# Kernel optimization log

Measured on AMD Instinct MI355X. Metric: run time of the kernel, lower is better.

## Reference

```python
import jax, jax.numpy as jnp
import numpy as np

EMBED_DIM = 256
H = 80
W = 80
N_HEADS = 8
N_POINTS = 4
B = 8


def sine_pe(C, h, w):
    # LoFTR-style PositionEncodingSine, returns [1, C, h, w]
    y_pos = jnp.cumsum(jnp.ones((h, w), jnp.float32), axis=0)[None]
    x_pos = jnp.cumsum(jnp.ones((h, w), jnp.float32), axis=1)[None]
    div = jnp.exp(jnp.arange(0, C // 2, 2, dtype=jnp.float32) * (-np.log(10000.0) / (C // 2)))[:, None, None]
    pe = jnp.zeros((C, h, w), jnp.float32)
    pe = pe.at[0::4].set(jnp.sin(x_pos * div))
    pe = pe.at[1::4].set(jnp.cos(x_pos * div))
    pe = pe.at[2::4].set(jnp.sin(y_pos * div))
    pe = pe.at[3::4].set(jnp.cos(y_pos * div))
    return pe[None]


def make_reference_points(h, w):
    # Faithful to the original (W-major flatten, (col, row) stacking)
    gr = np.linspace(0, 1, w)
    gc = np.linspace(0, 1, h)
    R, Cg = np.meshgrid(gr, gc, indexing='ij')  # (w, h)
    ref = np.stack((Cg, R), -1).reshape(-1, 2)  # [w*h, 2]
    return jnp.asarray(ref, jnp.float32)


def setup_inputs():
    key = jax.random.key(0)
    ks = jax.random.split(key, 8)
    C = EMBED_DIM
    s = 1.0 / np.sqrt(C)
    return {
        'query': jax.random.normal(ks[0], (B, C, H, W), jnp.float32),
        'value': jax.random.normal(ks[1], (B, C, H, W), jnp.float32),
        'W_value': jax.random.normal(ks[2], (C, C), jnp.float32) * s,
        'b_value': jnp.zeros((C,), jnp.float32),
        'W_off': jax.random.normal(ks[3], (C, N_HEADS * N_POINTS * 2), jnp.float32) * 0.01,
        'b_off': jax.random.normal(ks[4], (N_HEADS * N_POINTS * 2,), jnp.float32) * 0.5,
        'W_attn': jax.random.normal(ks[5], (C, N_HEADS * N_POINTS), jnp.float32) * s,
        'b_attn': jnp.zeros((N_HEADS * N_POINTS,), jnp.float32),
        'W_out': jax.random.normal(ks[6], (C, C), jnp.float32) * s,
        'b_out': jnp.zeros((C,), jnp.float32),
    }


def _deform_attn_core(q, v, ref, W_off, b_off, W_attn, b_attn):
    # q: [B, Nq, C] queries; v: [B, H*W, C] projected values; ref: [Nq, 2]
    Bq, Nq, C = q.shape
    hd = C // N_HEADS
    off = (q @ W_off + b_off).reshape(Bq, Nq, N_HEADS, N_POINTS, 2)
    aw = jax.nn.softmax((q @ W_attn + b_attn).reshape(Bq, Nq, N_HEADS, N_POINTS), axis=-1)
    norm = jnp.array([W, H], jnp.float32)  # offset normalizer (W, H), num_levels=1
    loc = ref[None, :, None, None, :] + off / norm  # [B, Nq, Hn, P, 2], normalized (x, y)
    loc = loc.transpose(0, 2, 1, 3, 4)  # [B, Hn, Nq, P, 2]
    # grid_sample(align_corners=False, padding_mode='zeros'): pixel = loc*size - 0.5
    x = loc[..., 0] * W - 0.5
    y = loc[..., 1] * H - 0.5
    x0f = jnp.floor(x); y0f = jnp.floor(y)
    wx = x - x0f; wy = y - y0f
    x0 = x0f.astype(jnp.int32); y0 = y0f.astype(jnp.int32)
    vh = v.reshape(Bq, H * W, N_HEADS, hd).transpose(0, 2, 1, 3)  # [B, Hn, HW, hd]

    def gather(ix, iy):
        valid = (ix >= 0) & (ix < W) & (iy >= 0) & (iy < H)
        idx = jnp.clip(iy, 0, H - 1) * W + jnp.clip(ix, 0, W - 1)  # [B, Hn, Nq, P]
        g = jnp.take_along_axis(vh, idx.reshape(Bq, N_HEADS, -1, 1), axis=2)
        return g.reshape(Bq, N_HEADS, Nq, N_POINTS, hd) * valid[..., None].astype(v.dtype)

    samp = (gather(x0, y0) * ((1 - wx) * (1 - wy))[..., None]
            + gather(x0 + 1, y0) * (wx * (1 - wy))[..., None]
            + gather(x0, y0 + 1) * ((1 - wx) * wy)[..., None]
            + gather(x0 + 1, y0 + 1) * (wx * wy)[..., None])  # [B, Hn, Nq, P, hd]
    out = jnp.einsum('bhqpd,bhqp->bqhd', samp, aw.transpose(0, 2, 1, 3))
    return out.reshape(Bq, Nq, C)


def reference(query, value, W_value, b_value, W_off, b_off, W_attn, b_attn, W_out, b_out):
    pe = sine_pe(EMBED_DIM, H, W)
    q = query + pe
    qf = q.reshape(B, EMBED_DIM, H * W).transpose(0, 2, 1)      # [B, Nq, C]
    vf = value.reshape(B, EMBED_DIM, H * W).transpose(0, 2, 1)  # [B, Nv, C]
    vproj = vf @ W_value + b_value
    ref = make_reference_points(H, W)
    attn = _deform_attn_core(qf, vproj, ref, W_off, b_off, W_attn, b_attn)
    attn = attn @ W_out + b_out
    attn = attn + qf  # mmcv MSDeformAttn residual (dropout identity at eval)
    out_img = attn.transpose(0, 2, 1).reshape(B, EMBED_DIM, H, W)
    # nn.Upsample(size=(H, W), bilinear) on an (H, W) map is identity (need_downsample=False)
    return (out_img + value, out_img)
```

## Files before the change

### kernel.cpp

```cpp
#include <hip/hip_runtime.h>
#include <hip/hip_bf16.h>
#include <stdint.h>

#define HH 80
#define WW 80
#define NQ 6400
#define CD 256
#define BB 8
#define OUT_HALF 13107200
#define PE_NEG 0.0719557841560639f

typedef __attribute__((ext_vector_type(4))) float f32x4;
typedef __bf16 bf16_t;
typedef __attribute__((ext_vector_type(8))) __bf16 bf16x8;

using gp1_t = const __attribute__((address_space(1))) void*;
using lp3_t = __attribute__((address_space(3))) void*;

__device__ __forceinline__ void gload_lds16(const void* g, void* l) {
    __builtin_amdgcn_global_load_lds((gp1_t)g, (lp3_t)l, 16, 0, 0);
}

__global__ __launch_bounds__(256) void wprep_kernel(const float* __restrict__ Wv,
                                                    const float* __restrict__ Woff,
                                                    const float* __restrict__ Wattn,
                                                    const float* __restrict__ Wout,
                                                    bf16_t* __restrict__ WvT,
                                                    bf16_t* __restrict__ WoaT,
                                                    bf16_t* __restrict__ WoT) {
    int idx = blockIdx.x * 256 + threadIdx.x;
    if (idx < 65536) {
        int cp = idx >> 8, c = idx & 255;
        WvT[idx] = (bf16_t)Wv[c * 256 + cp];
        WoT[idx] = (bf16_t)Wout[c * 256 + cp];
    }
    if (idx < 96 * 256) {
        int j = idx >> 8, c = idx & 255;
        WoaT[idx] = (bf16_t)(j < 64 ? Woff[c * 64 + j] : Wattn[c * 32 + (j - 64)]);
    }
}

__global__ __launch_bounds__(256, 3) void gemm_vproj(const float* __restrict__ V,
                                                     const bf16_t* __restrict__ Y,
                                                     const float* __restrict__ bias,
                                                     bf16_t* __restrict__ D) {
    __shared__ __align__(16) bf16_t lx[128 * 72];
    __shared__ __align__(16) bf16_t ly[128 * 64];
    int b = blockIdx.x & 7;
    int nloc = (blockIdx.x >> 3) * 128;
    int m0 = b * NQ + nloc;
    int c0 = blockIdx.y * 128;
    const float* src = V + (size_t)b * CD * NQ + nloc;
    int tid = threadIdx.x, wv = tid >> 6, ln = tid & 63;
    f32x4 acc[4][4] = {};
    int wr = (wv >> 1) * 64, wc = (wv & 1) * 64;
    int nl = tid & 31;
    for (int kt = 0; kt < 4; ++kt) {
#pragma unroll
        for (int q8 = 0; q8 < 4; ++q8) {
            int q = wv * 4 + q8;
            int row = q * 8 + (ln >> 3);
            int jj = (ln & 7) ^ (row & 7);
            gload_lds16((const char*)Y + ((size_t)(c0 + row)) * 512 + (size_t)kt * 128 + jj * 16,
                        (char*)ly + q * 1024);
        }
#pragma unroll
        for (int i = 0; i < 4; ++i) {
            int kp = (tid >> 5) + i * 8;
            int k = kp * 2;
            const float* s0 = src + (size_t)(kt * 64 + k) * NQ;
#pragma unroll
            for (int l = 0; l < 4; ++l) {
                int n = nl + 32 * l;
                float v0 = s0[n];
                float v1 = s0[NQ + n];
                union { bf16_t h[2]; uint32_t u; } pk;
                pk.h[0] = (bf16_t)v0; pk.h[1] = (bf16_t)v1;
                *(uint32_t*)((char*)lx + n * 144 + k * 2) = pk.u;
            }
        }
        __syncthreads();
#pragma unroll
        for (int ks = 0; ks < 2; ++ks) {
            bf16x8 xa[4], yb[4];
#pragma unroll
            for (int i = 0; i < 4; i++) {
                int m = wr + i * 16 + (ln & 15);
                xa[i] = *(const bf16x8*)((const char*)lx + m * 144 + ks * 64 + (ln >> 4) * 16);
                int n = wc + i * 16 + (ln & 15);
                int cn = (ks * 4 + (ln >> 4)) ^ (n & 7);
                yb[i] = *(const bf16x8*)((const char*)ly + n * 128 + cn * 16);
            }
#pragma unroll
            for (int i = 0; i < 4; i++)
#pragma unroll
                for (int j = 0; j < 4; j++)
                    acc[i][j] = __builtin_amdgcn_mfma_f32_16x16x32_bf16(xa[i], yb[j], acc[i][j], 0, 0, 0);
        }
        __syncthreads();
    }
#pragma unroll
    for (int i = 0; i < 4; i++)
#pragma unroll
        for (int j = 0; j < 4; j++) {
            int col = c0 + wc + j * 16 + (ln & 15);
            float bv = bias[col];
#pragma unroll
            for (int rg = 0; rg < 4; rg++) {
                int row = m0 + wr + i * 16 + (ln >> 4) * 4 + rg;
                D[(size_t)row * 256 + col] = (bf16_t)(acc[i][j][rg] + bv);
            }
        }
}

__global__ __launch_bounds__(256, 3) void oa_sample(const float* __restrict__ Q,
                                                    const bf16_t* __restrict__ Y,
                                                    const float* __restrict__ boff,
                                                    const float* __restrict__ battn,
                                                    const bf16_t* __restrict__ vp,
                                                    bf16_t* __restrict__ samp) {
    __shared__ __align__(16) bf16_t lx[128 * 72];
    __shared__ __align__(16) bf16_t ly[96 * 64];
    __shared__ bf16_t oaT[128][100];
    int bid = blockIdx.x;
    int b = bid & 7;
    int nloc = (bid >> 3) * 128;
    int m0 = b * NQ + nloc;
    const float* src = Q + (size_t)b * CD * NQ + nloc;
    int tid = threadIdx.x, wv = tid >> 6, ln = tid & 63;
    f32x4 acc[2][6] = {};
    int nl = tid & 31;
    for (int kt = 0; kt < 4; ++kt) {
#pragma unroll
        for (int q3 = 0; q3 < 3; ++q3) {
            int q = wv * 3 + q3;
            int row = q * 8 + (ln >> 3);
            int jj = (ln & 7) ^ (row & 7);
            gload_lds16((const char*)Y + ((size_t)row) * 512 + (size_t)kt * 128 + jj * 16,
                        (char*)ly + q * 1024);
        }
#pragma unroll
        for (int i = 0; i < 4; ++i) {
            int kp = (tid >> 5) + i * 8;
            int k = kp * 2;
            int c = kt * 64 + k;
            float d = __expf((float)(2 * (c >> 2)) * -PE_NEG);
            const float* s0 = src + (size_t)c * NQ;
#pragma unroll
            for (int l = 0; l < 4; ++l) {
                int n = nl + 32 * l;
                int p = nloc + n;
                int h = p / WW, w = p - h * WW;
                float pos = (c & 2) ? (float)(h + 1) : (float)(w + 1);
                float sv, cv;
                __sincosf(pos * d, &sv, &cv);
                float v0 = s0[n] + sv;
                float v1 = s0[NQ + n] + cv;
                union { bf16_t hh[2]; uint32_t u; } pk;
                pk.hh[0] = (bf16_t)v0; pk.hh[1] = (bf16_t)v1;
                *(uint32_t*)((char*)lx + n * 144 + k * 2) = pk.u;
            }
        }
        __syncthreads();
#pragma unroll
        for (int ks = 0; ks < 2; ++ks) {
            bf16x8 xa[2], yb[6];
#pragma unroll
            for (int i = 0; i < 2; i++) {
                int m = wv * 32 + i * 16 + (ln & 15);
                xa[i] = *(const bf16x8*)((const char*)lx + m * 144 + ks * 64 + (ln >> 4) * 16);
            }
#pragma unroll
            for (int j = 0; j < 6; j++) {
                int n = j * 16 + (ln & 15);
                int cn = (ks * 4 + (ln >> 4)) ^ (n & 7);
                yb[j] = *(const bf16x8*)((const char*)ly + n * 128 + cn * 16);
            }
#pragma unroll
            for (int i = 0; i < 2; i++)
#pragma unroll
                for (int j = 0; j < 6; j++)
                    acc[i][j] = __builtin_amdgcn_mfma_f32_16x16x32_bf16(xa[i], yb[j], acc[i][j], 0, 0, 0);
        }
        __syncthreads();
    }
#pragma unroll
    for (int i = 0; i < 2; i++)
#pragma unroll
        for (int j = 0; j < 6; j++) {
            int col = j * 16 + (ln & 15);
            float bv = col < 64 ? boff[col] : battn[col - 64];
#pragma unroll
            for (int rg = 0; rg < 4; rg++) {
                int rloc = wv * 32 + i * 16 + (ln >> 4) * 4 + rg;
                oaT[rloc][col] = (bf16_t)(acc[i][j][rg] + bv);
            }
        }
    __syncthreads();
    int h = (tid >> 1) & 7, sh = tid & 1;
    const bf16_t* vb = vp + (size_t)b * NQ * CD + h * 32 + sh * 16;
#pragma unroll
    for (int rnd = 0; rnd < 8; ++rnd) {
        int q = rnd * 16 + (tid >> 4);
        int n = nloc + q;
        const bf16_t* sq = oaT[q];
        float l0 = (float)sq[64 + h * 4 + 0], l1 = (float)sq[64 + h * 4 + 1];
        float l2 = (float)sq[64 + h * 4 + 2], l3 = (float)sq[64 + h * 4 + 3];
        float mx = fmaxf(fmaxf(l0, l1), fmaxf(l2, l3));
        float e0 = __expf(l0 - mx), e1 = __expf(l1 - mx), e2 = __expf(l2 - mx), e3 = __expf(l3 - mx);
        float inv = 1.f / (e0 + e1 + e2 + e3);
        float aw[4] = {e0 * inv, e1 * inv, e2 * inv, e3 * inv};
        float xb = (float)(n % WW) * (80.f / 79.f) - 0.5f;
        float yb = (float)(n / WW) * (80.f / 79.f) - 0.5f;
        float wgt[16];
        int idx[16];
#pragma unroll
        for (int p = 0; p < 4; p++) {
            float x = xb + (float)sq[h * 8 + p * 2];
            float y = yb + (float)sq[h * 8 + p * 2 + 1];
            float x0f = floorf(x), y0f = floorf(y);
            float wx = x - x0f, wy = y - y0f;
            int ix = (int)x0f, iy = (int)y0f;
            bool vx0 = (unsigned)ix < (unsigned)WW, vx1 = (unsigned)(ix + 1) < (unsigned)WW;
            bool vy0 = (unsigned)iy < (unsigned)HH, vy1 = (unsigned)(iy + 1) < (unsigned)HH;
            int cx0 = min(max(ix, 0), WW - 1), cx1 = min(max(ix + 1, 0), WW - 1);
            int cy0 = min(max(iy, 0), HH - 1), cy1 = min(max(iy + 1, 0), HH - 1);
            float ap = aw[p];
            wgt[p * 4 + 0] = (vx0 && vy0) ? ap * (1.f - wx) * (1.f - wy) : 0.f;
            wgt[p * 4 + 1] = (vx1 && vy0) ? ap * wx * (1.f - wy) : 0.f;
            wgt[p * 4 + 2] = (vx0 && vy1) ? ap * (1.f - wx) * wy : 0.f;
            wgt[p * 4 + 3] = (vx1 && vy1) ? ap * wx * wy : 0.f;
            idx[p * 4 + 0] = cy0 * WW + cx0;
            idx[p * 4 + 1] = cy0 * WW + cx1;
            idx[p * 4 + 2] = cy1 * WW + cx0;
            idx[p * 4 + 3] = cy1 * WW + cx1;
        }
        float fac[16];
#pragma unroll
        for (int j = 0; j < 16; j++) fac[j] = 0.f;
#pragma unroll
        for (int pc = 0; pc < 16; ++pc) {
            const bf16x8* p8 = (const bf16x8*)(vb + (size_t)idx[pc] * CD);
            bf16x8 v0 = p8[0], v1 = p8[1];
            float w = wgt[pc];
#pragma unroll
            for (int j = 0; j < 8; j++) fac[j] += (float)v0[j] * w;
#pragma unroll
            for (int j = 0; j < 8; j++) fac[8 + j] += (float)v1[j] * w;
        }
        bf16x8 o0, o1;
#pragma unroll
        for (int j = 0; j < 8; j++) { o0[j] = (bf16_t)fac[j]; o1[j] = (bf16_t)fac[8 + j]; }
        bf16x8* dst = (bf16x8*)(samp + (size_t)(m0 + q) * CD + h * 32 + sh * 16);
        dst[0] = o0;
        dst[1] = o1;
    }
}

__global__ __launch_bounds__(256, 4) void gemm_out(const bf16_t* __restrict__ X,
                                                   const bf16_t* __restrict__ Y,
                                                   const float* __restrict__ bout,
                                                   const float* __restrict__ query,
                                                   const float* __restrict__ value,
                                                   float* __restrict__ out) {
    __shared__ __align__(16) char smem[32768];
    bf16_t* lx = (bf16_t*)smem;
    bf16_t* ly = (bf16_t*)(smem + 16384);
    float* tile = (float*)smem;
    int m0 = blockIdx.x * 128;
    int b = blockIdx.y & 7;
    int nb = (blockIdx.y >> 3) * 128;
    int n0 = b * NQ + nb;
    int tid = threadIdx.x, wv = tid >> 6, ln = tid & 63;
    f32x4 acc[4][4] = {};
    int wr = (wv >> 1) * 64, wc = (wv & 1) * 64;
    for (int kt = 0; kt < 4; ++kt) {
#pragma unroll
        for (int q8 = 0; q8 < 4; ++q8) {
            int q = wv * 4 + q8;
            int row = q * 8 + (ln >> 3);
            int jj = (ln & 7) ^ (row & 7);
            gload_lds16((const char*)X + ((size_t)(m0 + row)) * 512 + (size_t)kt * 128 + jj * 16,
                        (char*)lx + q * 1024);
            gload_lds16((const char*)Y + ((size_t)(n0 + row)) * 512 + (size_t)kt * 128 + jj * 16,
                        (char*)ly + q * 1024);
        }
        __syncthreads();
#pragma unroll
        for (int ks = 0; ks < 2; ++ks) {
            bf16x8 xa[4], yb[4];
#pragma unroll
            for (int i = 0; i < 4; i++) {
                int m = wr + i * 16 + (ln & 15);
                int ch = (ks * 4 + (ln >> 4)) ^ (m & 7);
                xa[i] = *(const bf16x8*)((const char*)lx + m * 128 + ch * 16);
                int n = wc + i * 16 + (ln & 15);
                int cn = (ks * 4 + (ln >> 4)) ^ (n & 7);
                yb[i] = *(const bf16x8*)((const char*)ly + n * 128 + cn * 16);
            }
#pragma unroll
            for (int i = 0; i < 4; i++)
#pragma unroll
                for (int j = 0; j < 4; j++)
                    acc[i][j] = __builtin_amdgcn_mfma_f32_16x16x32_bf16(xa[i], yb[j], acc[i][j], 0, 0, 0);
        }
        __syncthreads();
    }
    const float* qp = query + (size_t)b * CD * NQ;
    const float* vp = value + (size_t)b * CD * NQ;
    float* o0 = out + (size_t)b * CD * NQ;
    float* o1 = out + OUT_HALF + (size_t)b * CD * NQ;
#pragma unroll
    for (int pass = 0; pass < 2; ++pass) {
        if ((wv >> 1) == pass) {
#pragma unroll
            for (int i = 0; i < 4; i++)
#pragma unroll
                for (int j = 0; j < 4; j++) {
                    int c = wc + j * 16 + (ln & 15);
#pragma unroll
                    for (int rg = 0; rg < 4; rg++) {
                        int r = i * 16 + (ln >> 4) * 4 + rg;
                        tile[r * 128 + c] = acc[i][j][rg] + bout[m0 + pass * 64 + r];
                    }
                }
        }
        __syncthreads();
        int g4 = (ln & 31) * 4;
        int rb = wv * 16 + (ln >> 5);
#pragma unroll
        for (int jj = 0; jj < 8; ++jj) {
            int r = rb + jj * 2;
            int crow = m0 + pass * 64 + r;
            size_t off = (size_t)crow * NQ + nb + g4;
            f32x4 tv = *(const f32x4*)&tile[r * 128 + g4];
            f32x4 qv = *(const f32x4*)(qp + off);
            f32x4 vv = *(const f32x4*)(vp + off);
            float d = __expf((float)(2 * (crow >> 2)) * -PE_NEG);
            bool useY = (crow & 2) != 0, odd = (crow & 1) != 0;
            f32x4 pv;
#pragma unroll
            for (int e = 0; e < 4; ++e) {
                int n = nb + g4 + e;
                int hh = n / WW, ww = n - hh * WW;
                float pos = useY ? (float)(hh + 1) : (float)(ww + 1);
                float sv, cv;
                __sincosf(pos * d, &sv, &cv);
                pv[e] = odd ? cv : sv;
            }
            f32x4 o1v = tv + qv + pv;
            *(f32x4*)(o1 + off) = o1v;
            *(f32x4*)(o0 + off) = o1v + vv;
        }
        __syncthreads();
    }
}

extern "C" void kernel_launch(void* const* d_in, const int* in_sizes, int n_in,
                              void* d_out, int out_size, void* d_ws, size_t ws_size,
                              hipStream_t stream) {
    const float* query   = (const float*)d_in[0];
    const float* value   = (const float*)d_in[1];
    const float* W_value = (const float*)d_in[2];
    const float* b_value = (const float*)d_in[3];
    const float* W_off   = (const float*)d_in[4];
    const float* b_off   = (const float*)d_in[5];
    const float* W_attn  = (const float*)d_in[6];
    const float* b_attn  = (const float*)d_in[7];
    const float* W_out   = (const float*)d_in[8];
    const float* b_out   = (const float*)d_in[9];
    float* out = (float*)d_out;
    char* ws = (char*)d_ws;

    bf16_t* WvT   = (bf16_t*)(ws + 0);
    bf16_t* WoT   = (bf16_t*)(ws + 131072);
    bf16_t* WoaT  = (bf16_t*)(ws + 262144);
    bf16_t* vprojB= (bf16_t*)(ws + 311296);
    bf16_t* samp  = (bf16_t*)(ws + 26525696);

    wprep_kernel<<<256, 256, 0, stream>>>(W_value, W_off, W_attn, W_out, WvT, WoaT, WoT);
    gemm_vproj<<<dim3(400, 2), 256, 0, stream>>>(value, WvT, b_value, vprojB);
    oa_sample<<<400, 256, 0, stream>>>(query, WoaT, b_off, b_attn, vprojB, samp);
    gemm_out<<<dim3(2, 400), 256, 0, stream>>>(WoT, samp, b_out, query, value, out);
}
```

Before: 112.7 us.

## Fuse deformable sampling with output projection and epilogue in one kernel

Merges the offset/attention projection and bilinear sampling kernel with the output-projection GEMM and residual epilogue. Each block now handles 64 queries and keeps the sampled features in swizzled LDS instead of writing them to a global bf16 buffer and reading them back. This removes a kernel launch and the global round trip of the intermediate tensor. In exchange, every block reloads the full W_out, uses more LDS (about 67KB, occupancy bound 2), and runs a smaller per-block tile.

```diff
diff --git a/kernel.cpp b/kernel.cpp
--- a/kernel.cpp
+++ b/kernel.cpp
@@ -113,246 +113,241 @@
         }
 }
 
-__global__ __launch_bounds__(256, 3) void oa_sample(const float* __restrict__ Q,
-                                                    const bf16_t* __restrict__ Y,
-                                                    const float* __restrict__ boff,
-                                                    const float* __restrict__ battn,
-                                                    const bf16_t* __restrict__ vp,
-                                                    bf16_t* __restrict__ samp) {
-    __shared__ __align__(16) bf16_t lx[128 * 72];
-    __shared__ __align__(16) bf16_t ly[96 * 64];
-    __shared__ bf16_t oaT[128][100];
+__global__ __launch_bounds__(256, 2) void oa_sample_out(
+        const float* __restrict__ Q,
+        const bf16_t* __restrict__ Woa,
+        const float* __restrict__ boff,
+        const float* __restrict__ battn,
+        const bf16_t* __restrict__ vp,
+        const bf16_t* __restrict__ WoT,
+        const float* __restrict__ bout,
+        const float* __restrict__ value,
+        float* __restrict__ out) {
+    __shared__ __align__(16) char smem[67072];
+    char* sampL = smem;
+    bf16_t* lx = (bf16_t*)(smem + 32768);
+    bf16_t* ly = (bf16_t*)(smem + 41984);
+    bf16_t* wx = (bf16_t*)(smem + 32768);
+    float* tile = (float*)(smem + 32768);
+    bf16_t* oaT = (bf16_t*)(smem + 54272);
+
     int bid = blockIdx.x;
     int b = bid & 7;
-    int nloc = (bid >> 3) * 128;
-    int m0 = b * NQ + nloc;
+    int nloc = (bid >> 3) * 64;
+    int tid = threadIdx.x, wv = tid >> 6, ln = tid & 63;
     const float* src = Q + (size_t)b * CD * NQ + nloc;
-    int tid = threadIdx.x, wv = tid >> 6, ln = tid & 63;
-    f32x4 acc[2][6] = {};
     int nl = tid & 31;
-    for (int kt = 0; kt < 4; ++kt) {
-#pragma unroll
-        for (int q3 = 0; q3 < 3; ++q3) {
-            int q = wv * 3 + q3;
-            int row = q * 8 + (ln >> 3);
-            int jj = (ln & 7) ^ (row & 7);
-            gload_lds16((const char*)Y + ((size_t)row) * 512 + (size_t)kt * 128 + jj * 16,
-                        (char*)ly + q * 1024);
-        }
-#pragma unroll
-        for (int i = 0; i < 4; ++i) {
-            int kp = (tid >> 5) + i * 8;
-            int k = kp * 2;
-            int c = kt * 64 + k;
-            float d = __expf((float)(2 * (c >> 2)) * -PE_NEG);
-            const float* s0 = src + (size_t)c * NQ;
-#pragma unroll
-            for (int l = 0; l < 4; ++l) {
-                int n = nl + 32 * l;
-                int p = nloc + n;
-                int h = p / WW, w = p - h * WW;
-                float pos = (c & 2) ? (float)(h + 1) : (float)(w + 1);
-                float sv, cv;
-                __sincosf(pos * d, &sv, &cv);
-                float v0 = s0[n] + sv;
-                float v1 = s0[NQ + n] + cv;
-                union { bf16_t hh[2]; uint32_t u; } pk;
-                pk.hh[0] = (bf16_t)v0; pk.hh[1] = (bf16_t)v1;
-                *(uint32_t*)((char*)lx + n * 144 + k * 2) = pk.u;
-            }
-        }
-        __syncthreads();
-#pragma unroll
-        for (int ks = 0; ks < 2; ++ks) {
-            bf16x8 xa[2], yb[6];
-#pragma unroll
-            for (int i = 0; i < 2; i++) {
-                int m = wv * 32 + i * 16 + (ln & 15);
-                xa[i] = *(const bf16x8*)((const char*)lx + m * 144 + ks * 64 + (ln >> 4) * 16);
-            }
-#pragma unroll
-            for (int j = 0; j < 6; j++) {
-                int n = j * 16 + (ln & 15);
-                int cn = (ks * 4 + (ln >> 4)) ^ (n & 7);
-                yb[j] = *(const bf16x8*)((const char*)ly + n * 128 + cn * 16);
-            }
-#pragma unroll
-            for (int i = 0; i < 2; i++)
+
+    {
+        f32x4 acc[1][6] = {};
+        for (int kt = 0; kt < 4; ++kt) {
+#pragma unroll
+            for (int q3 = 0; q3 < 3; ++q3) {
+                int q = wv * 3 + q3;
+                int row = q * 8 + (ln >> 3);
+                int jj = (ln & 7) ^ (row & 7);
+                gload_lds16((const char*)Woa + ((size_t)row) * 512 + (size_t)kt * 128 + jj * 16,
+                            (char*)ly + q * 1024);
+            }
+#pragma unroll
+            for (int i = 0; i < 4; ++i) {
+                int kp = (tid >> 5) + i * 8;
+                int k = kp * 2;
+                int c = kt * 64 + k;
+                float d = __expf((float)(2 * (c >> 2)) * -PE_NEG);
+                const float* s0 = src + (size_t)c * NQ;
+#pragma unroll
+                for (int l = 0; l < 2; ++l) {
+                    int n = nl + 32 * l;
+                    int p = nloc + n;
+                    int h = p / WW, w = p - h * WW;
+                    float pos = (c & 2) ? (float)(h + 1) : (float)(w + 1);
+                    float sv, cv;
+                    __sincosf(pos * d, &sv, &cv);
+                    float v0 = s0[n] + sv;
+                    float v1 = s0[NQ + n] + cv;
+                    union { bf16_t hh[2]; uint32_t u; } pk;
+                    pk.hh[0] = (bf16_t)v0; pk.hh[1] = (bf16_t)v1;
+                    *(uint32_t*)((char*)lx + n * 144 + k * 2) = pk.u;
+                }
+            }
+            __syncthreads();
+#pragma unroll
+            for (int ks = 0; ks < 2; ++ks) {
+                bf16x8 xa, yb[6];
+                int m = wv * 16 + (ln & 15);
+                xa = *(const bf16x8*)((const char*)lx + m * 144 + ks * 64 + (ln >> 4) * 16);
+#pragma unroll
+                for (int j = 0; j < 6; j++) {
+                    int n = j * 16 + (ln & 15);
+                    int cn = (ks * 4 + (ln >> 4)) ^ (n & 7);
+                    yb[j] = *(const bf16x8*)((const char*)ly + n * 128 + cn * 16);
+                }
 #pragma unroll
                 for (int j = 0; j < 6; j++)
-                    acc[i][j] = __builtin_amdgcn_mfma_f32_16x16x32_bf16(xa[i], yb[j], acc[i][j], 0, 0, 0);
-        }
-        __syncthreads();
-    }
-#pragma unroll
-    for (int i = 0; i < 2; i++)
+                    acc[0][j] = __builtin_amdgcn_mfma_f32_16x16x32_bf16(xa, yb[j], acc[0][j], 0, 0, 0);
+            }
+            __syncthreads();
+        }
 #pragma unroll
         for (int j = 0; j < 6; j++) {
             int col = j * 16 + (ln & 15);
             float bv = col < 64 ? boff[col] : battn[col - 64];
 #pragma unroll
             for (int rg = 0; rg < 4; rg++) {
-                int rloc = wv * 32 + i * 16 + (ln >> 4) * 4 + rg;
-                oaT[rloc][col] = (bf16_t)(acc[i][j][rg] + bv);
-            }
-        }
+                int rloc = wv * 16 + (ln >> 4) * 4 + rg;
+                oaT[rloc * 100 + col] = (bf16_t)(acc[0][j][rg] + bv);
+            }
+        }
+    }
     __syncthreads();
-    int h = (tid >> 1) & 7, sh = tid & 1;
-    const bf16_t* vb = vp + (size_t)b * NQ * CD + h * 32 + sh * 16;
-#pragma unroll
-    for (int rnd = 0; rnd < 8; ++rnd) {
-        int q = rnd * 16 + (tid >> 4);
-        int n = nloc + q;
-        const bf16_t* sq = oaT[q];
-        float l0 = (float)sq[64 + h * 4 + 0], l1 = (float)sq[64 + h * 4 + 1];
-        float l2 = (float)sq[64 + h * 4 + 2], l3 = (float)sq[64 + h * 4 + 3];
-        float mx = fmaxf(fmaxf(l0, l1), fmaxf(l2, l3));
-        float e0 = __expf(l0 - mx), e1 = __expf(l1 - mx), e2 = __expf(l2 - mx), e3 = __expf(l3 - mx);
-        float inv = 1.f / (e0 + e1 + e2 + e3);
-        float aw[4] = {e0 * inv, e1 * inv, e2 * inv, e3 * inv};
-        float xb = (float)(n % WW) * (80.f / 79.f) - 0.5f;
-        float yb = (float)(n / WW) * (80.f / 79.f) - 0.5f;
-        float wgt[16];
-        int idx[16];
-#pragma unroll
-        for (int p = 0; p < 4; p++) {
-            float x = xb + (float)sq[h * 8 + p * 2];
-            float y = yb + (float)sq[h * 8 + p * 2 + 1];
-            float x0f = floorf(x), y0f = floorf(y);
-            float wx = x - x0f, wy = y - y0f;
-            int ix = (int)x0f, iy = (int)y0f;
-            bool vx0 = (unsigned)ix < (unsigned)WW, vx1 = (unsigned)(ix + 1) < (unsigned)WW;
-            bool vy0 = (unsigned)iy < (unsigned)HH, vy1 = (unsigned)(iy + 1) < (unsigned)HH;
-            int cx0 = min(max(ix, 0), WW - 1), cx1 = min(max(ix + 1, 0), WW - 1);
-            int cy0 = min(max(iy, 0), HH - 1), cy1 = min(max(iy + 1, 0), HH - 1);
-            float ap = aw[p];
-            wgt[p * 4 + 0] = (vx0 && vy0) ? ap * (1.f - wx) * (1.f - wy) : 0.f;
-            wgt[p * 4 + 1] = (vx1 && vy0) ? ap * wx * (1.f - wy) : 0.f;
-            wgt[p * 4 + 2] = (vx0 && vy1) ? ap * (1.f - wx) * wy : 0.f;
-            wgt[p * 4 + 3] = (vx1 && vy1) ? ap * wx * wy : 0.f;
-            idx[p * 4 + 0] = cy0 * WW + cx0;
-            idx[p * 4 + 1] = cy0 * WW + cx1;
-            idx[p * 4 + 2] = cy1 * WW + cx0;
-            idx[p * 4 + 3] = cy1 * WW + cx1;
-        }
-        float fac[16];
-#pragma unroll
-        for (int j = 0; j < 16; j++) fac[j] = 0.f;
-#pragma unroll
-        for (int pc = 0; pc < 16; ++pc) {
-            const bf16x8* p8 = (const bf16x8*)(vb + (size_t)idx[pc] * CD);
-            bf16x8 v0 = p8[0], v1 = p8[1];
-            float w = wgt[pc];
-#pragma unroll
-            for (int j = 0; j < 8; j++) fac[j] += (float)v0[j] * w;
-#pragma unroll
-            for (int j = 0; j < 8; j++) fac[8 + j] += (float)v1[j] * w;
-        }
-        bf16x8 o0, o1;
-#pragma unroll
-        for (int j = 0; j < 8; j++) { o0[j] = (bf16_t)fac[j]; o1[j] = (bf16_t)fac[8 + j]; }
-        bf16x8* dst = (bf16x8*)(samp + (size_t)(m0 + q) * CD + h * 32 + sh * 16);
-        dst[0] = o0;
-        dst[1] = o1;
-    }
-}
-
-__global__ __launch_bounds__(256, 4) void gemm_out(const bf16_t* __restrict__ X,
-                                                   const bf16_t* __restrict__ Y,
-                                                   const float* __restrict__ bout,
-                                                   const float* __restrict__ query,
-                                                   const float* __restrict__ value,
-                                                   float* __restrict__ out) {
-    __shared__ __align__(16) char smem[32768];
-    bf16_t* lx = (bf16_t*)smem;
-    bf16_t* ly = (bf16_t*)(smem + 16384);
-    float* tile = (float*)smem;
-    int m0 = blockIdx.x * 128;
-    int b = blockIdx.y & 7;
-    int nb = (blockIdx.y >> 3) * 128;
-    int n0 = b * NQ + nb;
-    int tid = threadIdx.x, wv = tid >> 6, ln = tid & 63;
-    f32x4 acc[4][4] = {};
-    int wr = (wv >> 1) * 64, wc = (wv & 1) * 64;
-    for (int kt = 0; kt < 4; ++kt) {
-#pragma unroll
-        for (int q8 = 0; q8 < 4; ++q8) {
-            int q = wv * 4 + q8;
-            int row = q * 8 + (ln >> 3);
-            int jj = (ln & 7) ^ (row & 7);
-            gload_lds16((const char*)X + ((size_t)(m0 + row)) * 512 + (size_t)kt * 128 + jj * 16,
-                        (char*)lx + q * 1024);
-            gload_lds16((const char*)Y + ((size_t)(n0 + row)) * 512 + (size_t)kt * 128 + jj * 16,
-                        (char*)ly + q * 1024);
-        }
-        __syncthreads();
-#pragma unroll
-        for (int ks = 0; ks < 2; ++ks) {
-            bf16x8 xa[4], yb[4];
-#pragma unroll
-            for (int i = 0; i < 4; i++) {
-                int m = wr + i * 16 + (ln & 15);
-                int ch = (ks * 4 + (ln >> 4)) ^ (m & 7);
-                xa[i] = *(const bf16x8*)((const char*)lx + m * 128 + ch * 16);
-                int n = wc + i * 16 + (ln & 15);
-                int cn = (ks * 4 + (ln >> 4)) ^ (n & 7);
-                yb[i] = *(const bf16x8*)((const char*)ly + n * 128 + cn * 16);
-            }
-#pragma unroll
-            for (int i = 0; i < 4; i++)
-#pragma unroll
-                for (int j = 0; j < 4; j++)
-                    acc[i][j] = __builtin_amdgcn_mfma_f32_16x16x32_bf16(xa[i], yb[j], acc[i][j], 0, 0, 0);
-        }
-        __syncthreads();
-    }
-    const float* qp = query + (size_t)b * CD * NQ;
-    const float* vp = value + (size_t)b * CD * NQ;
-    float* o0 = out + (size_t)b * CD * NQ;
-    float* o1 = out + OUT_HALF + (size_t)b * CD * NQ;
-#pragma unroll
-    for (int pass = 0; pass < 2; ++pass) {
-        if ((wv >> 1) == pass) {
-#pragma unroll
-            for (int i = 0; i < 4; i++)
-#pragma unroll
-                for (int j = 0; j < 4; j++) {
-                    int c = wc + j * 16 + (ln & 15);
-#pragma unroll
-                    for (int rg = 0; rg < 4; rg++) {
-                        int r = i * 16 + (ln >> 4) * 4 + rg;
-                        tile[r * 128 + c] = acc[i][j][rg] + bout[m0 + pass * 64 + r];
+
+    {
+        int h = (tid >> 1) & 7, sh = tid & 1;
+        const bf16_t* vb = vp + (size_t)b * NQ * CD + h * 32 + sh * 16;
+#pragma unroll
+        for (int rnd = 0; rnd < 4; ++rnd) {
+            int q = rnd * 16 + (tid >> 4);
+            int n = nloc + q;
+            const bf16_t* sq = oaT + q * 100;
+            float l0 = (float)sq[64 + h * 4 + 0], l1 = (float)sq[64 + h * 4 + 1];
+            float l2 = (float)sq[64 + h * 4 + 2], l3 = (float)sq[64 + h * 4 + 3];
+            float mx = fmaxf(fmaxf(l0, l1), fmaxf(l2, l3));
+            float e0 = __expf(l0 - mx), e1 = __expf(l1 - mx), e2 = __expf(l2 - mx), e3 = __expf(l3 - mx);
+            float inv = 1.f / (e0 + e1 + e2 + e3);
+            float aw[4] = {e0 * inv, e1 * inv, e2 * inv, e3 * inv};
+            float xb = (float)(n % WW) * (80.f / 79.f) - 0.5f;
+            float yb = (float)(n / WW) * (80.f / 79.f) - 0.5f;
+            float wgt[16];
+            int idx[16];
+#pragma unroll
+            for (int p = 0; p < 4; p++) {
+                float x = xb + (float)sq[h * 8 + p * 2];
+                float y = yb + (float)sq[h * 8 + p * 2 + 1];
+                float x0f = floorf(x), y0f = floorf(y);
+                float wx_ = x - x0f, wy_ = y - y0f;
+                int ix = (int)x0f, iy = (int)y0f;
+                bool vx0 = (unsigned)ix < (unsigned)WW, vx1 = (unsigned)(ix + 1) < (unsigned)WW;
+                bool vy0 = (unsigned)iy < (unsigned)HH, vy1 = (unsigned)(iy + 1) < (unsigned)HH;
+                int cx0 = min(max(ix, 0), WW - 1), cx1 = min(max(ix + 1, 0), WW - 1);
+                int cy0 = min(max(iy, 0), HH - 1), cy1 = min(max(iy + 1, 0), HH - 1);
+                float ap = aw[p];
+                wgt[p * 4 + 0] = (vx0 && vy0) ? ap * (1.f - wx_) * (1.f - wy_) : 0.f;
+                wgt[p * 4 + 1] = (vx1 && vy0) ? ap * wx_ * (1.f - wy_) : 0.f;
+                wgt[p * 4 + 2] = (vx0 && vy1) ? ap * (1.f - wx_) * wy_ : 0.f;
+                wgt[p * 4 + 3] = (vx1 && vy1) ? ap * wx_ * wy_ : 0.f;
+                idx[p * 4 + 0] = cy0 * WW + cx0;
+                idx[p * 4 + 1] = cy0 * WW + cx1;
+                idx[p * 4 + 2] = cy1 * WW + cx0;
+                idx[p * 4 + 3] = cy1 * WW + cx1;
+            }
+            float fac[16];
+#pragma unroll
+            for (int j = 0; j < 16; j++) fac[j] = 0.f;
+#pragma unroll
+            for (int pc = 0; pc < 16; ++pc) {
+                const bf16x8* p8 = (const bf16x8*)(vb + (size_t)idx[pc] * CD);
+                bf16x8 v0 = p8[0], v1 = p8[1];
+                float w = wgt[pc];
+#pragma unroll
+                for (int j = 0; j < 8; j++) fac[j] += (float)v0[j] * w;
+#pragma unroll
+                for (int j = 0; j < 8; j++) fac[8 + j] += (float)v1[j] * w;
+            }
+            bf16x8 o0, o1;
+#pragma unroll
+            for (int j = 0; j < 8; j++) { o0[j] = (bf16_t)fac[j]; o1[j] = (bf16_t)fac[8 + j]; }
+            int c0 = 4 * h + 2 * sh;
+            *(bf16x8*)(sampL + q * 512 + ((c0 ^ (q & 7)) * 16)) = o0;
+            *(bf16x8*)(sampL + q * 512 + (((c0 + 1) ^ (q & 7)) * 16)) = o1;
+        }
+    }
+    __syncthreads();
+
+    const float* qp = Q + (size_t)b * CD * NQ;
+    const float* vvp = value + (size_t)b * CD * NQ;
+    float* o0p = out + (size_t)b * CD * NQ;
+    float* o1p = out + OUT_HALF + (size_t)b * CD * NQ;
+    for (int p = 0; p < 2; ++p) {
+        int cb = p * 128;
+        f32x4 acc[4][2] = {};
+        for (int kt = 0; kt < 4; ++kt) {
+#pragma unroll
+            for (int q8 = 0; q8 < 4; ++q8) {
+                int q = wv * 4 + q8;
+                int row = q * 8 + (ln >> 3);
+                int jj = (ln & 7) ^ (row & 7);
+                gload_lds16((const char*)WoT + ((size_t)(cb + row)) * 512 + (size_t)kt * 128 + jj * 16,
+                            (char*)wx + q * 1024);
+            }
+            __syncthreads();
+#pragma unroll
+            for (int ks = 0; ks < 2; ++ks) {
+                bf16x8 xa[4], yb[2];
+#pragma unroll
+                for (int i = 0; i < 4; i++) {
+                    int m = (wv >> 1) * 64 + i * 16 + (ln & 15);
+                    int ch = (ks * 4 + (ln >> 4)) ^ (m & 7);
+                    xa[i] = *(const bf16x8*)((const char*)wx + m * 128 + ch * 16);
+                }
+#pragma unroll
+                for (int j = 0; j < 2; j++) {
+                    int nr = (wv & 1) * 32 + j * 16 + (ln & 15);
+                    int cj = kt * 8 + ks * 4 + (ln >> 4);
+                    yb[j] = *(const bf16x8*)(sampL + nr * 512 + ((cj ^ (nr & 7)) * 16));
+                }
+#pragma unroll
+                for (int i = 0; i < 4; i++)
+#pragma unroll
+                    for (int j = 0; j < 2; j++)
+                        acc[i][j] = __builtin_amdgcn_mfma_f32_16x16x32_bf16(xa[i], yb[j], acc[i][j], 0, 0, 0);
+            }
+            __syncthreads();
+        }
+#pragma unroll
+        for (int hp = 0; hp < 2; ++hp) {
+            if ((wv >> 1) == hp) {
+#pragma unroll
+                for (int i = 0; i < 4; i++)
+#pragma unroll
+                    for (int j = 0; j < 2; j++) {
+                        int c = (wv & 1) * 32 + j * 16 + (ln & 15);
+#pragma unroll
+                        for (int rg = 0; rg < 4; rg++) {
+                            int r = i * 16 + (ln >> 4) * 4 + rg;
+                            tile[r * 68 + c] = acc[i][j][rg] + bout[cb + hp * 64 + r];
+                        }
                     }
-                }
-        }
-        __syncthreads();
-        int g4 = (ln & 31) * 4;
-        int rb = wv * 16 + (ln >> 5);
-#pragma unroll
-        for (int jj = 0; jj < 8; ++jj) {
-            int r = rb + jj * 2;
-            int crow = m0 + pass * 64 + r;
-            size_t off = (size_t)crow * NQ + nb + g4;
-            f32x4 tv = *(const f32x4*)&tile[r * 128 + g4];
-            f32x4 qv = *(const f32x4*)(qp + off);
-            f32x4 vv = *(const f32x4*)(vp + off);
-            float d = __expf((float)(2 * (crow >> 2)) * -PE_NEG);
-            bool useY = (crow & 2) != 0, odd = (crow & 1) != 0;
-            f32x4 pv;
-#pragma unroll
-            for (int e = 0; e < 4; ++e) {
-                int n = nb + g4 + e;
-                int hh = n / WW, ww = n - hh * WW;
-                float pos = useY ? (float)(hh + 1) : (float)(ww + 1);
-                float sv, cv;
-                __sincosf(pos * d, &sv, &cv);
-                pv[e] = odd ? cv : sv;
-            }
-            f32x4 o1v = tv + qv + pv;
-            *(f32x4*)(o1 + off) = o1v;
-            *(f32x4*)(o0 + off) = o1v + vv;
-        }
-        __syncthreads();
+            }
+            __syncthreads();
+            int g4 = (tid & 15) * 4;
+            int rowbase = tid >> 4;
+#pragma unroll
+            for (int jj = 0; jj < 4; ++jj) {
+                int r = rowbase + jj * 16;
+                int crow = cb + hp * 64 + r;
+                size_t off = (size_t)crow * NQ + nloc + g4;
+                f32x4 tv = *(const f32x4*)&tile[r * 68 + g4];
+                f32x4 qv = *(const f32x4*)(qp + off);
+                f32x4 vv = *(const f32x4*)(vvp + off);
+                float d = __expf((float)(2 * (crow >> 2)) * -PE_NEG);
+                bool useY = (crow & 2) != 0, odd = (crow & 1) != 0;
+                f32x4 pv;
+#pragma unroll
+                for (int e = 0; e < 4; ++e) {
+                    int n = nloc + g4 + e;
+                    int hh = n / WW, ww = n - hh * WW;
+                    float pos = useY ? (float)(hh + 1) : (float)(ww + 1);
+                    float sv, cv;
+                    __sincosf(pos * d, &sv, &cv);
+                    pv[e] = odd ? cv : sv;
+                }
+                f32x4 o1v = tv + qv + pv;
+                *(f32x4*)(o1p + off) = o1v;
+                *(f32x4*)(o0p + off) = o1v + vv;
+            }
+            __syncthreads();
+        }
     }
 }
 
@@ -376,10 +371,9 @@
     bf16_t* WoT   = (bf16_t*)(ws + 131072);
     bf16_t* WoaT  = (bf16_t*)(ws + 262144);
     bf16_t* vprojB= (bf16_t*)(ws + 311296);
-    bf16_t* samp  = (bf16_t*)(ws + 26525696);
 
     wprep_kernel<<<256, 256, 0, stream>>>(W_value, W_off, W_attn, W_out, WvT, WoaT, WoT);
     gemm_vproj<<<dim3(400, 2), 256, 0, stream>>>(value, WvT, b_value, vprojB);
-    oa_sample<<<400, 256, 0, stream>>>(query, WoaT, b_off, b_attn, vprojB, samp);
-    gemm_out<<<dim3(2, 400), 256, 0, stream>>>(WoT, samp, b_out, query, value, out);
-}
+    oa_sample_out<<<800, 256, 0, stream>>>(query, WoaT, b_off, b_attn, vprojB,
+                                           WoT, b_out, value, out);
+}
```

After: 102.4 us. -9.1%, faster.
